# Optimization experiments

Measured on AMD Instinct MI355X. Metric: run time of the kernel, lower is better.

The kernel has to match this reference:

```python
import jax, jax.numpy as jnp
import numpy as np

TOP_K = 2


def setup_inputs() -> dict:
    key = jax.random.key(0)
    k1, k2, k3, k4, k5 = jax.random.split(key, 5)
    B, S, H, F, E = 2, 2048, 1024, 4096, 8
    scale = 0.02
    return {
        "hidden_states": jax.random.normal(k1, (B, S, H), dtype=jnp.float32),
        "w_gate": jax.random.normal(k2, (H, E), dtype=jnp.float32) * scale,
        "w_gate_proj": jax.random.normal(k3, (E, H, F), dtype=jnp.float32) * scale,
        "w_up_proj": jax.random.normal(k4, (E, H, F), dtype=jnp.float32) * scale,
        "w_down_proj": jax.random.normal(k5, (E, F, H), dtype=jnp.float32) * scale,
    }


def reference(hidden_states, w_gate, w_gate_proj, w_up_proj, w_down_proj):
    B, S, H = hidden_states.shape
    E = w_gate_proj.shape[0]
    x = hidden_states.reshape(-1, H)  # [T, H]

    # Router: softmax in float32, then top-k (NOT renormalized, matching source).
    router_logits = x @ w_gate  # [T, E]
    routing_probs = jax.nn.softmax(router_logits.astype(jnp.float32), axis=-1)
    routing_weights, selected_experts = jax.lax.top_k(routing_probs, TOP_K)  # [T, k]
    routing_weights = routing_weights.astype(x.dtype)

    out = jnp.zeros_like(x)
    # Small fixed loop over experts; per-token weight is zero for unrouted
    # tokens, so the masked dense computation is mathematically identical to
    # the gather/index_add dispatch in the source.
    for e in range(E):
        w_e = jnp.sum(routing_weights * (selected_experts == e), axis=-1)  # [T]
        h = jax.nn.silu(x @ w_gate_proj[e]) * (x @ w_up_proj[e])  # [T, F]
        out = out + (h @ w_down_proj[e]) * w_e[:, None]
    return out.reshape(B, S, H)
```

## Files before the change

### kernel.cpp

```cpp
#include <hip/hip_runtime.h>
#include <hip/hip_bf16.h>

#define T_TOK 4096
#define HDIM  1024
#define FDIM  4096
#define NEXP  8
#define CAP   4096
#define MAXWL 128
#define OBR   (2 * T_TOK + 128)

typedef __attribute__((ext_vector_type(8))) short short8;
typedef __attribute__((ext_vector_type(4))) float floatx4;
typedef __attribute__((ext_vector_type(4))) float float4v;
typedef __attribute__((ext_vector_type(4))) unsigned short ushort4v;

__device__ __forceinline__ unsigned short f2bf(float f) {
    union { float f; unsigned int u; } v; v.f = f;
    unsigned int u = v.u;
    u += 0x7fffu + ((u >> 16) & 1u);
    return (unsigned short)(u >> 16);
}

__device__ __forceinline__ void gl2lds16(const void* g, void* l) {
    __builtin_amdgcn_global_load_lds(
        (const __attribute__((address_space(1))) unsigned int*)g,
        (__attribute__((address_space(3))) unsigned int*)l,
        16, 0, 0);
}

__global__ void k_transpose_cast(const float* __restrict__ src, unsigned short* __restrict__ dst,
                                 int R, int C) {
    __shared__ float tile[64][65];
    size_t base = (size_t)blockIdx.z * (size_t)R * (size_t)C;
    int c0 = blockIdx.x * 64, r0 = blockIdx.y * 64;
    int lx = threadIdx.x & 15, ly = threadIdx.x >> 4;
#pragma unroll
    for (int i = 0; i < 4; ++i) {
        int rr = i * 16 + ly;
        float4v v = *(const float4v*)(src + base + (size_t)(r0 + rr) * C + c0 + lx * 4);
        tile[rr][lx * 4 + 0] = v[0]; tile[rr][lx * 4 + 1] = v[1];
        tile[rr][lx * 4 + 2] = v[2]; tile[rr][lx * 4 + 3] = v[3];
    }
    __syncthreads();
#pragma unroll
    for (int i = 0; i < 4; ++i) {
        int cc = i * 16 + ly;
        ushort4v o = { f2bf(tile[lx * 4 + 0][cc]), f2bf(tile[lx * 4 + 1][cc]),
                       f2bf(tile[lx * 4 + 2][cc]), f2bf(tile[lx * 4 + 3][cc]) };
        *(ushort4v*)(dst + base + (size_t)(c0 + cc) * R + r0 + lx * 4) = o;
    }
}

__global__ void k_transpose_cast2(const float* __restrict__ s0, const float* __restrict__ s1,
                                  unsigned short* __restrict__ d0, unsigned short* __restrict__ d1) {
    const int R = HDIM, C = FDIM;
    __shared__ float tile[64][65];
    int m = blockIdx.z >> 3, zz = blockIdx.z & 7;
    const float* src = (m ? s1 : s0);
    unsigned short* dst = (m ? d1 : d0);
    size_t base = (size_t)zz * (size_t)R * (size_t)C;
    int c0 = blockIdx.x * 64, r0 = blockIdx.y * 64;
    int lx = threadIdx.x & 15, ly = threadIdx.x >> 4;
#pragma unroll
    for (int i = 0; i < 4; ++i) {
        int rr = i * 16 + ly;
        float4v v = *(const float4v*)(src + base + (size_t)(r0 + rr) * C + c0 + lx * 4);
        tile[rr][lx * 4 + 0] = v[0]; tile[rr][lx * 4 + 1] = v[1];
        tile[rr][lx * 4 + 2] = v[2]; tile[rr][lx * 4 + 3] = v[3];
    }
    __syncthreads();
#pragma unroll
    for (int i = 0; i < 4; ++i) {
        int cc = i * 16 + ly;
        ushort4v o = { f2bf(tile[lx * 4 + 0][cc]), f2bf(tile[lx * 4 + 1][cc]),
                       f2bf(tile[lx * 4 + 2][cc]), f2bf(tile[lx * 4 + 3][cc]) };
        *(ushort4v*)(dst + base + (size_t)(c0 + cc) * R + r0 + lx * 4) = o;
    }
}

__global__ void k_router(const float* __restrict__ x, const float* __restrict__ wgate,
                         unsigned short* __restrict__ xb,
                         int* __restrict__ counts, int* __restrict__ ltok,
                         float* __restrict__ lwt, int* __restrict__ tslot) {
    int lane = threadIdx.x & 63;
    int tok = blockIdx.x * 4 + (threadIdx.x >> 6);
    const float* xr = x + (size_t)tok * HDIM;
    unsigned short* xbr = xb + (size_t)tok * HDIM;
    float acc[NEXP];
#pragma unroll
    for (int e = 0; e < NEXP; ++e) acc[e] = 0.f;
    for (int it = 0; it < HDIM / 256; ++it) {
        int h0 = it * 256 + lane * 4;
        float4v xv = *(const float4v*)(xr + h0);
        ushort4v xo = { f2bf(xv[0]), f2bf(xv[1]), f2bf(xv[2]), f2bf(xv[3]) };
        *(ushort4v*)(xbr + h0) = xo;
#pragma unroll
        for (int j = 0; j < 4; ++j) {
            float4v w0 = *(const float4v*)(wgate + (size_t)(h0 + j) * NEXP);
            float4v w1 = *(const float4v*)(wgate + (size_t)(h0 + j) * NEXP + 4);
            float xs = xv[j];
            acc[0] += xs * w0[0]; acc[1] += xs * w0[1];
            acc[2] += xs * w0[2]; acc[3] += xs * w0[3];
            acc[4] += xs * w1[0]; acc[5] += xs * w1[1];
            acc[6] += xs * w1[2]; acc[7] += xs * w1[3];
        }
    }
#pragma unroll
    for (int off = 32; off >= 1; off >>= 1)
#pragma unroll
        for (int e = 0; e < NEXP; ++e)
            acc[e] += __shfl_xor(acc[e], off, 64);
    if (lane == 0) {
        float m = acc[0];
#pragma unroll
        for (int e = 1; e < NEXP; ++e) m = fmaxf(m, acc[e]);
        float p[NEXP], s = 0.f;
#pragma unroll
        for (int e = 0; e < NEXP; ++e) { p[e] = __expf(acc[e] - m); s += p[e]; }
        float inv = 1.f / s;
#pragma unroll
        for (int e = 0; e < NEXP; ++e) p[e] *= inv;
        int e0 = 0; float b0 = p[0];
#pragma unroll
        for (int e = 1; e < NEXP; ++e) if (p[e] > b0) { b0 = p[e]; e0 = e; }
        int e1 = -1; float b1 = -1.f;
#pragma unroll
        for (int e = 0; e < NEXP; ++e) if (e != e0 && p[e] > b1) { b1 = p[e]; e1 = e; }
        int p0 = atomicAdd(&counts[e0], 1);
        ltok[e0 * CAP + p0] = tok; lwt[e0 * CAP + p0] = b0;
        int p1 = atomicAdd(&counts[e1], 1);
        ltok[e1 * CAP + p1] = tok; lwt[e1 * CAP + p1] = b1;
        tslot[tok * 2]     = (e0 << 16) | p0;
        tslot[tok * 2 + 1] = (e1 << 16) | p1;
    }
}

__global__ void k_prefix(const int* __restrict__ counts, int* __restrict__ offs,
                         int* __restrict__ wl, int* __restrict__ nwl) {
    if (threadIdx.x == 0) {
        int s = 0;
#pragma unroll
        for (int e = 0; e < NEXP; ++e) { offs[e] = s; s += counts[e]; }
        int n = 0;
        for (int e = 0; e < NEXP; ++e)
            for (int r = 0; r * 128 < counts[e] && n < MAXWL; ++r)
                wl[n++] = (e << 8) | r;
        nwl[0] = n;
    }
}

__global__ __launch_bounds__(256, 4)
void k_gemm1(const unsigned short* __restrict__ xb,
             const unsigned short* __restrict__ wgt,
             const unsigned short* __restrict__ wut,
             const int* __restrict__ counts, const int* __restrict__ offs,
             const int* __restrict__ ltok,
             const int* __restrict__ wl, const int* __restrict__ nwl,
             unsigned short* __restrict__ hbuf)
{
    const int bid = blockIdx.x;
    const int xcd = bid & 7;
    const int jj  = bid >> 3;
    const int fhi = jj & 7;
    const int by  = jj >> 3;
    if (by >= nwl[0]) return;
    const int ftile = xcd + 8 * fhi;
    const int w = wl[by];
    const int e = w >> 8, rowtile = w & 255;
    const int M = counts[e];

    __shared__ __align__(16) unsigned short lA[2][128 * 32];
    __shared__ __align__(16) unsigned short lBg[2][64 * 32];
    __shared__ __align__(16) unsigned short lBu[2][64 * 32];
    __shared__ int stok[128];

    const int t = threadIdx.x;
    const int wave = t >> 6, lane = t & 63;

    if (t < 128) {
        int i = rowtile * 128 + t;
        stok[t] = (i < M) ? ltok[e * CAP + i] : ltok[e * CAP];
    }
    __syncthreads();

    const int r0 = t >> 2, k8 = t & 3;
    const int sw0 = (k8 ^ ((r0 >> 1) & 3)) * 8;
    const unsigned short* pA0 = xb + (size_t)stok[r0] * HDIM + sw0;
    const unsigned short* pA1 = xb + (size_t)stok[r0 + 64] * HDIM + sw0;
    const size_t wbase = (size_t)e * FDIM * HDIM + (size_t)(ftile * 64) * HDIM;
    const unsigned short* pG0 = wgt + wbase + (size_t)r0 * HDIM + sw0;
    const unsigned short* pU0 = wut + wbase + (size_t)r0 * HDIM + sw0;

    const int wm = wave >> 1, wn = wave & 1;
    const int fr = lane & 15, kg = lane >> 4;
    const int cswz = (kg ^ ((fr >> 1) & 3)) * 8;

    floatx4 accg[4][2], accu[4][2];
#pragma unroll
    for (int mi = 0; mi < 4; ++mi)
#pragma unroll
        for (int ni = 0; ni < 2; ++ni) {
            floatx4 z = {0.f, 0.f, 0.f, 0.f};
            accg[mi][ni] = z; accu[mi][ni] = z;
        }

    auto stage = [&](int b) {
        gl2lds16(pA0, &lA[b][wave * 512]);        pA0 += 32;
        gl2lds16(pA1, &lA[b][2048 + wave * 512]); pA1 += 32;
        gl2lds16(pG0, &lBg[b][wave * 512]);       pG0 += 32;
        gl2lds16(pU0, &lBu[b][wave * 512]);       pU0 += 32;
    };
    auto compute = [&](int b) {
        short8 a[4], g[2], u[2];
#pragma unroll
        for (int mi = 0; mi < 4; ++mi)
            a[mi] = *(const short8*)&lA[b][(wm * 64 + mi * 16 + fr) * 32 + cswz];
#pragma unroll
        for (int ni = 0; ni < 2; ++ni) {
            g[ni] = *(const short8*)&lBg[b][(wn * 32 + ni * 16 + fr) * 32 + cswz];
            u[ni] = *(const short8*)&lBu[b][(wn * 32 + ni * 16 + fr) * 32 + cswz];
        }
#pragma unroll
        for (int mi = 0; mi < 4; ++mi)
#pragma unroll
            for (int ni = 0; ni < 2; ++ni) {
                accg[mi][ni] = __builtin_amdgcn_mfma_f32_16x16x32_bf16(a[mi], g[ni], accg[mi][ni], 0, 0, 0);
                accu[mi][ni] = __builtin_amdgcn_mfma_f32_16x16x32_bf16(a[mi], u[ni], accu[mi][ni], 0, 0, 0);
            }
    };

    stage(0);
    __syncthreads();
#pragma unroll 1
    for (int it = 0; it < 16; ++it) {
        stage(1);
        compute(0);
        __syncthreads();
        if (it < 15) stage(0);
        compute(1);
        __syncthreads();
    }

    const int hrow0 = offs[e] + rowtile * 128;
#pragma unroll
    for (int mi = 0; mi < 4; ++mi)
#pragma unroll
        for (int ni = 0; ni < 2; ++ni) {
            int c = ftile * 64 + wn * 32 + ni * 16 + fr;
#pragma unroll
            for (int r = 0; r < 4; ++r) {
                int rr = wm * 64 + mi * 16 + kg * 4 + r;
                if (rowtile * 128 + rr < M) {
                    float g = accg[mi][ni][r];
                    float val = (g / (1.f + __expf(-g))) * accu[mi][ni][r];
                    hbuf[(size_t)(hrow0 + rr) * FDIM + c] = f2bf(val);
                }
            }
        }
}

__global__ __launch_bounds__(256, 4)
void k_gemm2(const unsigned short* __restrict__ hbuf,
             const unsigned short* __restrict__ wdt,
             const int* __restrict__ counts, const int* __restrict__ offs,
             const float* __restrict__ lwt,
             const int* __restrict__ wl, const int* __restrict__ nwl,
             float* __restrict__ obuf)
{
    const int bid = blockIdx.x;
    const int htile = bid & 7;
    const int jj = bid >> 3;
    const int khalf = jj & 1;
    const int by = jj >> 1;
    if (by >= nwl[0]) return;
    const int w = wl[by];
    const int e = w >> 8, rowtile = w & 255;
    const int M = counts[e];

    __shared__ __align__(16) unsigned short lA[2][128 * 32];
    __shared__ __align__(16) unsigned short lB[2][128 * 32];
    __shared__ float swt[128];

    const int t = threadIdx.x;
    const int wave = t >> 6, lane = t & 63;

    if (t < 128) {
        int i = rowtile * 128 + t;
        swt[t] = (i < M) ? lwt[e * CAP + i] : 0.f;
    }

    const int row0 = offs[e] + rowtile * 128;
    const int r0 = t >> 2, k8 = t & 3;
    const int kofs = khalf * (FDIM / 2);
    const int sw0 = (k8 ^ ((r0 >> 1) & 3)) * 8;
    const unsigned short* pA0 = hbuf + (size_t)(row0 + r0) * FDIM + kofs + sw0;
    const unsigned short* pA1 = hbuf + (size_t)(row0 + 64 + r0) * FDIM + kofs + sw0;
    const size_t wb = (size_t)e * HDIM * FDIM + (size_t)(htile * 128) * FDIM;
    const unsigned short* pB0 = wdt + wb + (size_t)r0 * FDIM + kofs + sw0;
    const unsigned short* pB1 = wdt + wb + (size_t)(64 + r0) * FDIM + kofs + sw0;

    const int wm = wave >> 1, wn = wave & 1;
    const int fr = lane & 15, kg = lane >> 4;
    const int cswz = (kg ^ ((fr >> 1) & 3)) * 8;

    floatx4 acc[4][4];
#pragma unroll
    for (int mi = 0; mi < 4; ++mi)
#pragma unroll
        for (int ni = 0; ni < 4; ++ni) {
            floatx4 z = {0.f, 0.f, 0.f, 0.f};
            acc[mi][ni] = z;
        }

    auto stage = [&](int b) {
        gl2lds16(pA0, &lA[b][wave * 512]);        pA0 += 32;
        gl2lds16(pA1, &lA[b][2048 + wave * 512]); pA1 += 32;
        gl2lds16(pB0, &lB[b][wave * 512]);        pB0 += 32;
        gl2lds16(pB1, &lB[b][2048 + wave * 512]); pB1 += 32;
    };
    auto compute = [&](int b) {
        short8 a[4], bb[4];
#pragma unroll
        for (int mi = 0; mi < 4; ++mi)
            a[mi] = *(const short8*)&lA[b][(wm * 64 + mi * 16 + fr) * 32 + cswz];
#pragma unroll
        for (int ni = 0; ni < 4; ++ni)
            bb[ni] = *(const short8*)&lB[b][(wn * 64 + ni * 16 + fr) * 32 + cswz];
#pragma unroll
        for (int mi = 0; mi < 4; ++mi)
#pragma unroll
            for (int ni = 0; ni < 4; ++ni)
                acc[mi][ni] = __builtin_amdgcn_mfma_f32_16x16x32_bf16(a[mi], bb[ni], acc[mi][ni], 0, 0, 0);
    };

    stage(0);
    __syncthreads();
#pragma unroll 1
    for (int it = 0; it < 32; ++it) {
        stage(1);
        compute(0);
        __syncthreads();
        if (it < 31) stage(0);
        compute(1);
        __syncthreads();
    }

    float* ob = obuf + (size_t)khalf * OBR * HDIM;
#pragma unroll
    for (int mi = 0; mi < 4; ++mi)
#pragma unroll
        for (int ni = 0; ni < 4; ++ni) {
            int c = htile * 128 + wn * 64 + ni * 16 + fr;
#pragma unroll
            for (int r = 0; r < 4; ++r) {
                int rr = wm * 64 + mi * 16 + kg * 4 + r;
                if (rowtile * 128 + rr < M)
                    ob[(size_t)(row0 + rr) * HDIM + c] = acc[mi][ni][r] * swt[rr];
            }
        }
}

__global__ void k_combine(const float* __restrict__ obuf, const int* __restrict__ tslot,
                          const int* __restrict__ offs, float* __restrict__ out) {
    int gid = blockIdx.x * 256 + threadIdx.x;
    int tok = gid >> 8;
    int c = (gid & 255) * 4;
    int s0 = tslot[tok * 2], s1 = tslot[tok * 2 + 1];
    size_t r0 = (size_t)(offs[s0 >> 16] + (s0 & 0xFFFF));
    size_t r1 = (size_t)(offs[s1 >> 16] + (s1 & 0xFFFF));
    float4v v00 = *(const float4v*)(obuf + r0 * HDIM + c);
    float4v v01 = *(const float4v*)(obuf + ((size_t)OBR + r0) * HDIM + c);
    float4v v10 = *(const float4v*)(obuf + r1 * HDIM + c);
    float4v v11 = *(const float4v*)(obuf + ((size_t)OBR + r1) * HDIM + c);
    float4v s = v00 + v01 + v10 + v11;
    *(float4v*)(out + (size_t)tok * HDIM + c) = s;
}

extern "C" void kernel_launch(void* const* d_in, const int* in_sizes, int n_in,
                              void* d_out, int out_size, void* d_ws, size_t ws_size,
                              hipStream_t stream) {
    const float* x     = (const float*)d_in[0];
    const float* wgate = (const float*)d_in[1];
    const float* wg    = (const float*)d_in[2];
    const float* wu    = (const float*)d_in[3];
    const float* wd    = (const float*)d_in[4];
    float* out = (float*)d_out;

    char* ws = (char*)d_ws;
    size_t off = 0;
    unsigned short* xb  = (unsigned short*)(ws + off); off += (size_t)T_TOK * HDIM * 2;
    unsigned short* wgt = (unsigned short*)(ws + off); off += (size_t)NEXP * FDIM * HDIM * 2;
    unsigned short* wut = (unsigned short*)(ws + off); off += (size_t)NEXP * FDIM * HDIM * 2;
    unsigned short* wdt = (unsigned short*)(ws + off); off += (size_t)NEXP * HDIM * FDIM * 2;
    unsigned short* hbuf= (unsigned short*)(ws + off); off += (size_t)OBR * FDIM * 2;
    int*   ltok   = (int*)(ws + off);   off += (size_t)NEXP * CAP * 4;
    float* lwt    = (float*)(ws + off); off += (size_t)NEXP * CAP * 4;
    int*   tslot  = (int*)(ws + off);   off += (size_t)T_TOK * 2 * 4;
    int*   counts = (int*)(ws + off);   off += 256;
    int*   offs   = (int*)(ws + off);   off += 256;
    int*   wl     = (int*)(ws + off);   off += MAXWL * 4;
    int*   nwl    = (int*)(ws + off);   off += 256;
    float* obuf = (float*)wgt;

    hipMemsetAsync(counts, 0, 32, stream);

    k_router<<<T_TOK / 4, 256, 0, stream>>>(x, wgate, xb, counts, ltok, lwt, tslot);
    k_transpose_cast2<<<dim3(FDIM / 64, HDIM / 64, 16), 256, 0, stream>>>(wg, wu, wgt, wut);
    k_transpose_cast<<<dim3(HDIM / 64, FDIM / 64, NEXP), 256, 0, stream>>>(wd, wdt, FDIM, HDIM);
    k_prefix<<<1, 64, 0, stream>>>(counts, offs, wl, nwl);
    k_gemm1<<<8 * 8 * 72, 256, 0, stream>>>(xb, wgt, wut, counts, offs, ltok, wl, nwl, hbuf);
    k_gemm2<<<8 * 2 * 72, 256, 0, stream>>>(hbuf, wdt, counts, offs, lwt, wl, nwl, obuf);
    k_combine<<<T_TOK * HDIM / 1024, 256, 0, stream>>>(obuf, tslot, offs, out);
}
```

Measured before the change: 827.5 us.

## Use 256-row tiles with 8-wave blocks and 4-way split-K in MoE GEMMs

Both expert GEMMs move from 128-row tiles with 4 waves to 256-row tiles with 8 waves, so each weight tile loaded into LDS is reused across twice as many tokens. GEMM2 now splits K four ways instead of two, which adds more fp32 partial buffers that the combine kernel must read and sum. The XCD-aware block swizzle in GEMM1 is dropped, and padded rows get more wasted work for small expert groups. LDS per block grows, which may limit occupancy.

```diff
diff --git a/kernel.cpp b/kernel.cpp
--- a/kernel.cpp
+++ b/kernel.cpp
@@ -6,8 +6,8 @@
 #define FDIM  4096
 #define NEXP  8
 #define CAP   4096
-#define MAXWL 128
-#define OBR   (2 * T_TOK + 128)
+#define NTMAX 64
+#define OBR   8192
 
 typedef __attribute__((ext_vector_type(8))) short short8;
 typedef __attribute__((ext_vector_type(4))) float floatx4;
@@ -143,13 +143,13 @@
         for (int e = 0; e < NEXP; ++e) { offs[e] = s; s += counts[e]; }
         int n = 0;
         for (int e = 0; e < NEXP; ++e)
-            for (int r = 0; r * 128 < counts[e] && n < MAXWL; ++r)
+            for (int r = 0; r * 256 < counts[e] && n < NTMAX; ++r)
                 wl[n++] = (e << 8) | r;
         nwl[0] = n;
     }
 }
 
-__global__ __launch_bounds__(256, 4)
+__global__ __launch_bounds__(512, 4)
 void k_gemm1(const unsigned short* __restrict__ xb,
              const unsigned short* __restrict__ wgt,
              const unsigned short* __restrict__ wut,
@@ -159,39 +159,38 @@
              unsigned short* __restrict__ hbuf)
 {
     const int bid = blockIdx.x;
-    const int xcd = bid & 7;
-    const int jj  = bid >> 3;
-    const int fhi = jj & 7;
-    const int by  = jj >> 3;
+    const int ftile = bid & 63;
+    const int by = bid >> 6;
     if (by >= nwl[0]) return;
-    const int ftile = xcd + 8 * fhi;
     const int w = wl[by];
     const int e = w >> 8, rowtile = w & 255;
     const int M = counts[e];
 
-    __shared__ __align__(16) unsigned short lA[2][128 * 32];
+    __shared__ __align__(16) unsigned short lA[2][256 * 32];
     __shared__ __align__(16) unsigned short lBg[2][64 * 32];
     __shared__ __align__(16) unsigned short lBu[2][64 * 32];
-    __shared__ int stok[128];
+    __shared__ int stok[256];
 
     const int t = threadIdx.x;
-    const int wave = t >> 6, lane = t & 63;
-
-    if (t < 128) {
-        int i = rowtile * 128 + t;
+    const int wv = t >> 6, lane = t & 63;
+
+    if (t < 256) {
+        int i = rowtile * 256 + t;
         stok[t] = (i < M) ? ltok[e * CAP + i] : ltok[e * CAP];
     }
     __syncthreads();
 
-    const int r0 = t >> 2, k8 = t & 3;
-    const int sw0 = (k8 ^ ((r0 >> 1) & 3)) * 8;
-    const unsigned short* pA0 = xb + (size_t)stok[r0] * HDIM + sw0;
-    const unsigned short* pA1 = xb + (size_t)stok[r0 + 64] * HDIM + sw0;
-    const size_t wbase = (size_t)e * FDIM * HDIM + (size_t)(ftile * 64) * HDIM;
-    const unsigned short* pG0 = wgt + wbase + (size_t)r0 * HDIM + sw0;
-    const unsigned short* pU0 = wut + wbase + (size_t)r0 * HDIM + sw0;
-
-    const int wm = wave >> 1, wn = wave & 1;
+    const int srow = wv * 16 + (lane >> 2);
+    const int k4 = lane & 3;
+    const int swA = (k4 ^ ((srow >> 1) & 3)) * 8;
+    const unsigned short* pA0 = xb + (size_t)stok[srow] * HDIM + swA;
+    const unsigned short* pA1 = xb + (size_t)stok[128 + srow] * HDIM + swA;
+    const int brow = (wv & 3) * 16 + (lane >> 2);
+    const int swB = (k4 ^ ((brow >> 1) & 3)) * 8;
+    const unsigned short* wsrc = (wv < 4) ? wgt : wut;
+    const unsigned short* pB = wsrc + ((size_t)e * FDIM + ftile * 64 + brow) * HDIM + swB;
+
+    const int wm = wv >> 1, wn = wv & 1;
     const int fr = lane & 15, kg = lane >> 4;
     const int cswz = (kg ^ ((fr >> 1) & 3)) * 8;
 
@@ -205,10 +204,11 @@
         }
 
     auto stage = [&](int b) {
-        gl2lds16(pA0, &lA[b][wave * 512]);        pA0 += 32;
-        gl2lds16(pA1, &lA[b][2048 + wave * 512]); pA1 += 32;
-        gl2lds16(pG0, &lBg[b][wave * 512]);       pG0 += 32;
-        gl2lds16(pU0, &lBu[b][wave * 512]);       pU0 += 32;
+        gl2lds16(pA0, &lA[b][wv * 512]);        pA0 += 32;
+        gl2lds16(pA1, &lA[b][4096 + wv * 512]); pA1 += 32;
+        gl2lds16(pB, (wv < 4) ? &lBg[b][(wv & 3) * 512]
+                              : &lBu[b][(wv & 3) * 512]);
+        pB += 32;
     };
     auto compute = [&](int b) {
         short8 a[4], g[2], u[2];
@@ -241,7 +241,7 @@
         __syncthreads();
     }
 
-    const int hrow0 = offs[e] + rowtile * 128;
+    const int hrow0 = offs[e] + rowtile * 256;
 #pragma unroll
     for (int mi = 0; mi < 4; ++mi)
 #pragma unroll
@@ -250,7 +250,7 @@
 #pragma unroll
             for (int r = 0; r < 4; ++r) {
                 int rr = wm * 64 + mi * 16 + kg * 4 + r;
-                if (rowtile * 128 + rr < M) {
+                if (rowtile * 256 + rr < M) {
                     float g = accg[mi][ni][r];
                     float val = (g / (1.f + __expf(-g))) * accu[mi][ni][r];
                     hbuf[(size_t)(hrow0 + rr) * FDIM + c] = f2bf(val);
@@ -259,7 +259,7 @@
         }
 }
 
-__global__ __launch_bounds__(256, 4)
+__global__ __launch_bounds__(512, 4)
 void k_gemm2(const unsigned short* __restrict__ hbuf,
              const unsigned short* __restrict__ wdt,
              const int* __restrict__ counts, const int* __restrict__ offs,
@@ -269,37 +269,37 @@
 {
     const int bid = blockIdx.x;
     const int htile = bid & 7;
-    const int jj = bid >> 3;
-    const int khalf = jj & 1;
-    const int by = jj >> 1;
+    const int kq = (bid >> 3) & 3;
+    const int by = bid >> 5;
     if (by >= nwl[0]) return;
     const int w = wl[by];
     const int e = w >> 8, rowtile = w & 255;
     const int M = counts[e];
 
-    __shared__ __align__(16) unsigned short lA[2][128 * 32];
+    __shared__ __align__(16) unsigned short lA[2][256 * 32];
     __shared__ __align__(16) unsigned short lB[2][128 * 32];
-    __shared__ float swt[128];
+    __shared__ float swt[256];
 
     const int t = threadIdx.x;
-    const int wave = t >> 6, lane = t & 63;
-
-    if (t < 128) {
-        int i = rowtile * 128 + t;
+    const int wv = t >> 6, lane = t & 63;
+
+    if (t < 256) {
+        int i = rowtile * 256 + t;
         swt[t] = (i < M) ? lwt[e * CAP + i] : 0.f;
     }
 
-    const int row0 = offs[e] + rowtile * 128;
-    const int r0 = t >> 2, k8 = t & 3;
-    const int kofs = khalf * (FDIM / 2);
-    const int sw0 = (k8 ^ ((r0 >> 1) & 3)) * 8;
-    const unsigned short* pA0 = hbuf + (size_t)(row0 + r0) * FDIM + kofs + sw0;
-    const unsigned short* pA1 = hbuf + (size_t)(row0 + 64 + r0) * FDIM + kofs + sw0;
-    const size_t wb = (size_t)e * HDIM * FDIM + (size_t)(htile * 128) * FDIM;
-    const unsigned short* pB0 = wdt + wb + (size_t)r0 * FDIM + kofs + sw0;
-    const unsigned short* pB1 = wdt + wb + (size_t)(64 + r0) * FDIM + kofs + sw0;
-
-    const int wm = wave >> 1, wn = wave & 1;
+    const int row0 = offs[e] + rowtile * 256;
+    const int srow = wv * 16 + (lane >> 2);
+    const int k4 = lane & 3;
+    const int sw = (k4 ^ ((srow >> 1) & 3)) * 8;
+    const int kofs = kq * (FDIM / 4);
+    const int ra0 = min(row0 + srow, OBR - 1);
+    const int ra1 = min(row0 + 128 + srow, OBR - 1);
+    const unsigned short* pA0 = hbuf + (size_t)ra0 * FDIM + kofs + sw;
+    const unsigned short* pA1 = hbuf + (size_t)ra1 * FDIM + kofs + sw;
+    const unsigned short* pB = wdt + ((size_t)e * HDIM + htile * 128 + srow) * FDIM + kofs + sw;
+
+    const int wm = wv >> 1, wn = wv & 1;
     const int fr = lane & 15, kg = lane >> 4;
     const int cswz = (kg ^ ((fr >> 1) & 3)) * 8;
 
@@ -313,10 +313,9 @@
         }
 
     auto stage = [&](int b) {
-        gl2lds16(pA0, &lA[b][wave * 512]);        pA0 += 32;
-        gl2lds16(pA1, &lA[b][2048 + wave * 512]); pA1 += 32;
-        gl2lds16(pB0, &lB[b][wave * 512]);        pB0 += 32;
-        gl2lds16(pB1, &lB[b][2048 + wave * 512]); pB1 += 32;
+        gl2lds16(pA0, &lA[b][wv * 512]);        pA0 += 32;
+        gl2lds16(pA1, &lA[b][4096 + wv * 512]); pA1 += 32;
+        gl2lds16(pB,  &lB[b][wv * 512]);        pB += 32;
     };
     auto compute = [&](int b) {
         short8 a[4], bb[4];
@@ -336,16 +335,16 @@
     stage(0);
     __syncthreads();
 #pragma unroll 1
-    for (int it = 0; it < 32; ++it) {
+    for (int it = 0; it < 16; ++it) {
         stage(1);
         compute(0);
         __syncthreads();
-        if (it < 31) stage(0);
+        if (it < 15) stage(0);
         compute(1);
         __syncthreads();
     }
 
-    float* ob = obuf + (size_t)khalf * OBR * HDIM;
+    float* ob = obuf + (size_t)kq * OBR * HDIM;
 #pragma unroll
     for (int mi = 0; mi < 4; ++mi)
 #pragma unroll
@@ -354,7 +353,7 @@
 #pragma unroll
             for (int r = 0; r < 4; ++r) {
                 int rr = wm * 64 + mi * 16 + kg * 4 + r;
-                if (rowtile * 128 + rr < M)
+                if (rowtile * 256 + rr < M)
                     ob[(size_t)(row0 + rr) * HDIM + c] = acc[mi][ni][r] * swt[rr];
             }
         }
@@ -368,11 +367,12 @@
     int s0 = tslot[tok * 2], s1 = tslot[tok * 2 + 1];
     size_t r0 = (size_t)(offs[s0 >> 16] + (s0 & 0xFFFF));
     size_t r1 = (size_t)(offs[s1 >> 16] + (s1 & 0xFFFF));
-    float4v v00 = *(const float4v*)(obuf + r0 * HDIM + c);
-    float4v v01 = *(const float4v*)(obuf + ((size_t)OBR + r0) * HDIM + c);
-    float4v v10 = *(const float4v*)(obuf + r1 * HDIM + c);
-    float4v v11 = *(const float4v*)(obuf + ((size_t)OBR + r1) * HDIM + c);
-    float4v s = v00 + v01 + v10 + v11;
+    float4v s = {0.f, 0.f, 0.f, 0.f};
+#pragma unroll
+    for (int q = 0; q < 4; ++q) {
+        s += *(const float4v*)(obuf + ((size_t)q * OBR + r0) * HDIM + c);
+        s += *(const float4v*)(obuf + ((size_t)q * OBR + r1) * HDIM + c);
+    }
     *(float4v*)(out + (size_t)tok * HDIM + c) = s;
 }
 
@@ -398,7 +398,7 @@
     int*   tslot  = (int*)(ws + off);   off += (size_t)T_TOK * 2 * 4;
     int*   counts = (int*)(ws + off);   off += 256;
     int*   offs   = (int*)(ws + off);   off += 256;
-    int*   wl     = (int*)(ws + off);   off += MAXWL * 4;
+    int*   wl     = (int*)(ws + off);   off += NTMAX * 4;
     int*   nwl    = (int*)(ws + off);   off += 256;
     float* obuf = (float*)wgt;
 
@@ -408,7 +408,7 @@
     k_transpose_cast2<<<dim3(FDIM / 64, HDIM / 64, 16), 256, 0, stream>>>(wg, wu, wgt, wut);
     k_transpose_cast<<<dim3(HDIM / 64, FDIM / 64, NEXP), 256, 0, stream>>>(wd, wdt, FDIM, HDIM);
     k_prefix<<<1, 64, 0, stream>>>(counts, offs, wl, nwl);
-    k_gemm1<<<8 * 8 * 72, 256, 0, stream>>>(xb, wgt, wut, counts, offs, ltok, wl, nwl, hbuf);
-    k_gemm2<<<8 * 2 * 72, 256, 0, stream>>>(hbuf, wdt, counts, offs, lwt, wl, nwl, obuf);
+    k_gemm1<<<64 * 40, 512, 0, stream>>>(xb, wgt, wut, counts, offs, ltok, wl, nwl, hbuf);
+    k_gemm2<<<32 * 40, 512, 0, stream>>>(hbuf, wdt, counts, offs, lwt, wl, nwl, obuf);
     k_combine<<<T_TOK * HDIM / 1024, 256, 0, stream>>>(obuf, tslot, offs, out);
 }
```

Result: no change. 827.6 us (+0.0%).
